# Kernel tuning notes

Hardware: AMD Instinct MI355X
Metric: run time of the kernel (lower is better)

The kernel has to match this reference:

```python
import jax, jax.numpy as jnp
import numpy as np

B, N, H, K, WIN = 512, 600, 256, 9, 129
AVG = 1.5
PAD = K // 2
PWIN = WIN + 2 * PAD  # padded window length


def setup_inputs() -> dict:
    key = jax.random.key(0)
    ks = jax.random.split(key, 8)
    tokens = jax.random.normal(ks[0], (B, N, H), dtype=jnp.float32)
    token_keys = jax.random.normal(ks[1], (B, H, N), dtype=jnp.float32)
    query = jax.random.normal(ks[2], (B, H), dtype=jnp.float32)
    num_tokens = jax.random.randint(ks[3], (B,), 300, N + 1, dtype=jnp.int32)
    tokens_mask = jnp.arange(N)[None, :] < num_tokens[:, None]
    u = jax.random.uniform(ks[4], (B,))
    window_start = (u * (num_tokens - WIN + 1).astype(jnp.float32)).astype(jnp.int32)
    alignment = jax.random.uniform(ks[5], (B, N + 2 * PAD), dtype=jnp.float32)
    cum_alignment = jax.random.uniform(ks[6], (B, N + 2 * PAD), dtype=jnp.float32) * 50.0
    conv_w = jax.random.normal(ks[7], (H, 2, K), dtype=jnp.float32) * 0.1
    conv_b = jnp.zeros((H,), dtype=jnp.float32)
    return dict(tokens=tokens, tokens_mask=tokens_mask, token_keys=token_keys,
                num_tokens=num_tokens, query=query, alignment=alignment,
                cum_alignment=cum_alignment, window_start=window_start,
                conv_w=conv_w, conv_b=conv_b)


def reference(tokens, tokens_mask, token_keys, num_tokens, query, alignment,
              cum_alignment, window_start, conv_w, conv_b):
    scale = jnp.sqrt(jnp.float32(H))
    idx = window_start[:, None] + jnp.arange(WIN)
    pidx = window_start[:, None] + jnp.arange(PWIN)        # [B, PWIN]
    mask_w = jnp.take_along_axis(tokens_mask, idx, axis=1)
    tokens_w = jnp.take_along_axis(tokens, idx[:, :, None], axis=1)
    keys_w = jnp.take_along_axis(token_keys, idx[:, None, :], axis=2)
    last_w = jnp.take_along_axis(alignment, pidx, axis=1)                  # [B, PWIN]
    cum_w = jnp.take_along_axis(cum_alignment, pidx, axis=1)               # [B, PWIN]
    position = jnp.stack([cum_w / AVG - 1.0, last_w * 2.0 - 1.0], axis=1)  # [B, 2, PWIN]
    position = jax.lax.stop_gradient(position)  # .detach() in torch
    feat = jax.lax.conv_general_dilated(position, conv_w, (1,), 'VALID',
                                        dimension_numbers=('NCH', 'OIH', 'NCH'))
    feat = feat + conv_b[None, :, None]
    keys = feat + keys_w
    score = jnp.einsum('bh,bhw->bw', query, keys) / scale
    score = jnp.where(mask_w, score, -jnp.inf)
    align_w = jax.nn.softmax(score, axis=1)
    context = jnp.einsum('bw,bwh->bh', align_w, tokens_w)                  # [B, H]
    b_idx = jnp.arange(B)[:, None]
    full_align = jnp.zeros_like(alignment).at[b_idx, idx + PAD].set(align_w)
    new_start = jnp.argmax(full_align, axis=1).astype(jnp.int32) - PWIN // 2
    new_start = jnp.maximum(window_start, new_start)
    new_start = jnp.minimum(new_start, num_tokens - WIN)
    new_start = jnp.maximum(new_start, 0)
    unpadded = full_align[:, PAD:-PAD]                                     # [B, N]
    return (context, unpadded, full_align, cum_alignment + full_align, new_start)
```

## Files before the change

kernel.cpp:

```cpp
#include <hip/hip_runtime.h>
#include <math.h>

#define BB   512
#define NN   600
#define HH   256
#define KS   9
#define WIN  129
#define PADW 4
#define PWIN 137
#define NP   608

__global__ __launch_bounds__(1024) void attn_kernel(
    const float* __restrict__ tokens,
    const float* __restrict__ token_keys,
    const int*   __restrict__ num_tokens,
    const float* __restrict__ query,
    const float* __restrict__ alignment,
    const float* __restrict__ cum_align,
    const int*   __restrict__ window_start,
    const float* __restrict__ conv_w,
    const float* __restrict__ conv_b,
    float* __restrict__ out)
{
  const int b    = blockIdx.x;
  const int t    = threadIdx.x;
  const int lane = t & 63;
  const int wv   = t >> 6;

  __shared__ float sq[HH];
  __shared__ float scw[HH * 18];
  __shared__ float scb[HH];
  __shared__ float p0[PWIN], p1[PWIN];
  __shared__ float cred[19][8];
  __shared__ float w128red[4];
  __shared__ float sqc[19];
  __shared__ float sS[8][130];
  __shared__ float salign[WIN];
  __shared__ int   cand[WIN];
  __shared__ __align__(16) float sctx[16][HH];
  __shared__ float s_m, s_sum;
  __shared__ int   s_arg;

  const int ws = window_start[b];
  const int nt = num_tokens[b];
  const float* Kb = token_keys + (size_t)b * (HH * NN);

  float qreg = 0.f;
  if (t < HH) {
    qreg = query[b * HH + t];
    sq[t] = qreg;
    scb[t] = conv_b[t];
  }
  #pragma unroll
  for (int i = 0; i < 5; ++i) {
    int j = t + i * 1024;
    if (j < HH * 18) scw[j] = conv_w[j];
  }
  if (t < PWIN) {
    p0[t] = cum_align[b * NP + ws + t] * (1.0f / 1.5f) - 1.0f;
    p1[t] = alignment[b * NP + ws + t] * 2.0f - 1.0f;
  }
  __syncthreads();

  if (t < 152) {
    const int j = t >> 3, seg = t & 7;
    const int h0 = seg * 32;
    float a = 0.f;
    if (j < 18) {
      #pragma unroll 8
      for (int h = 0; h < 32; ++h) a += sq[h0 + h] * scw[(h0 + h) * 18 + j];
    } else {
      #pragma unroll 8
      for (int h = 0; h < 32; ++h) a += sq[h0 + h] * scb[h0 + h];
    }
    cred[j][seg] = a;
  }

  if (t < HH) {
    float v = qreg * Kb[(size_t)t * NN + ws + 128];
    #pragma unroll
    for (int off = 32; off; off >>= 1) v += __shfl_xor(v, off, 64);
    if (lane == 0) w128red[wv] = v;
  }

  {
    const int hh   = wv & 7;
    const int wseg = wv >> 3;
    const int w    = wseg * 64 + lane;
    const float* Kp  = Kb + (size_t)(hh * 32) * NN + ws + w;
    const float* sqp = sq + hh * 32;
    float acc = 0.f;
    #pragma unroll 8
    for (int h = 0; h < 32; ++h) acc += sqp[h] * Kp[(size_t)h * NN];
    sS[hh][w] = acc;
  }
  __syncthreads();

  if (t < 19) {
    const float* c = cred[t];
    sqc[t] = ((c[0] + c[1]) + (c[2] + c[3])) + ((c[4] + c[5]) + (c[6] + c[7]));
  }
  __syncthreads();

  float sc = 0.f;
  if (t < WIN) {
    float dot;
    if (t < 128) {
      dot = 0.f;
      #pragma unroll
      for (int g = 0; g < 8; ++g) dot += sS[g][t];
    } else {
      dot = w128red[0] + w128red[1] + w128red[2] + w128red[3];
    }
    float f = sqc[18];
    #pragma unroll
    for (int k = 0; k < KS; ++k) f += sqc[k] * p0[t + k] + sqc[9 + k] * p1[t + k];
    sc = (dot + f) * 0.0625f;
    if (ws + t >= nt) sc = -INFINITY;
    salign[t] = sc;
  }
  __syncthreads();

  if (t < 64) {
    float m0 = fmaxf(salign[t], salign[t + 64]);
    if (t == 0) m0 = fmaxf(m0, salign[128]);
    #pragma unroll
    for (int off = 32; off; off >>= 1) m0 = fmaxf(m0, __shfl_xor(m0, off, 64));
    if (t == 0) s_m = m0;
  }
  __syncthreads();
  if (t < WIN) {
    float e = expf(sc - s_m);
    salign[t] = e;
    cand[t] = (sc == s_m) ? t : 0x7fffffff;
  }
  __syncthreads();
  if (t < 64) {
    float s0 = salign[t] + salign[t + 64] + ((t == 0) ? salign[128] : 0.f);
    int   c0 = min(cand[t], cand[t + 64]);
    if (t == 0) c0 = min(c0, cand[128]);
    #pragma unroll
    for (int off = 32; off; off >>= 1) {
      s0 += __shfl_xor(s0, off, 64);
      c0 = min(c0, __shfl_xor(c0, off, 64));
    }
    if (t == 0) { s_sum = s0; s_arg = c0; }
  }
  __syncthreads();
  const float inv = 1.0f / s_sum;
  if (t < WIN) salign[t] *= inv;
  __syncthreads();

  float* out0 = out;
  float* out1 = out0 + BB * HH;
  float* out2 = out1 + BB * NN;
  float* out3 = out2 + BB * NP;
  float* out4 = out3 + BB * NP;

  {
    const float* Tb = tokens + (size_t)b * (NN * HH) + (size_t)ws * HH;
    float4 acc = make_float4(0.f, 0.f, 0.f, 0.f);
    #pragma unroll
    for (int i = 0; i < 8; ++i) {
      const int w = wv + 16 * i;
      const float a = salign[w];
      const float4 v4 = ((const float4*)(Tb + (size_t)w * HH))[lane];
      acc.x += a * v4.x; acc.y += a * v4.y; acc.z += a * v4.z; acc.w += a * v4.w;
    }
    if (wv == 0) {
      const float a = salign[128];
      const float4 v4 = ((const float4*)(Tb + (size_t)128 * HH))[lane];
      acc.x += a * v4.x; acc.y += a * v4.y; acc.z += a * v4.z; acc.w += a * v4.w;
    }
    ((float4*)&sctx[wv][0])[lane] = acc;
  }
  __syncthreads();
  if (t < HH) {
    float c = 0.f;
    #pragma unroll
    for (int v = 0; v < 16; ++v) c += sctx[v][t];
    out0[b * HH + t] = c;
  }

  if (t < NN) {
    float v = (t >= ws && t <= ws + 128) ? salign[t - ws] : 0.f;
    out1[b * NN + t] = v;
  }
  if (t < NP) {
    float v = (t >= ws + PADW && t <= ws + PADW + 128) ? salign[t - ws - PADW] : 0.f;
    out2[b * NP + t] = v;
    out3[b * NP + t] = v + cum_align[b * NP + t];
  }
  if (t == 0) {
    int jstar = ws + PADW + s_arg;
    int ns = jstar - (PWIN / 2);
    ns = max(ws, ns);
    ns = min(ns, nt - WIN);
    ns = max(ns, 0);
    out4[b] = (float)ns;
  }
}

extern "C" void kernel_launch(void* const* d_in, const int* in_sizes, int n_in,
                              void* d_out, int out_size, void* d_ws, size_t ws_size,
                              hipStream_t stream) {
  const float* tokens       = (const float*)d_in[0];
  const float* token_keys   = (const float*)d_in[2];
  const int*   num_tokens   = (const int*)d_in[3];
  const float* query        = (const float*)d_in[4];
  const float* alignment    = (const float*)d_in[5];
  const float* cum_align    = (const float*)d_in[6];
  const int*   window_start = (const int*)d_in[7];
  const float* conv_w       = (const float*)d_in[8];
  const float* conv_b       = (const float*)d_in[9];

  attn_kernel<<<BB, 1024, 0, stream>>>(tokens, token_keys, num_tokens, query,
                                       alignment, cum_align, window_start,
                                       conv_w, conv_b, (float*)d_out);
}
```

Before: 512.1 us.

## Halve block size, drop smem conv weights, fuse softmax reductions, defer normalization

Moves from 1024-thread to 512-thread blocks with a launch bound of 512 threads and 8 blocks per CU, and redistributes the key-dot, context and output loops to match. Removes the per-block shared-memory staging of conv weights and bias, reading them straight from global memory instead, which shrinks shared memory and should allow more resident blocks. Merges the max, argmax, exp and sum steps into a single wavefront pass, removing several barriers. Applies the softmax normalization as a multiply at output time instead of a separate pass. Cumulative-alignment loads are issued early so their latency overlaps with compute. The cost is more serial work per thread and uncached global reads of conv weights per block.

```diff
diff --git a/kernel.cpp b/kernel.cpp
--- a/kernel.cpp
+++ b/kernel.cpp
@@ -10,7 +10,7 @@
 #define PWIN 137
 #define NP   608
 
-__global__ __launch_bounds__(1024) void attn_kernel(
+__global__ __launch_bounds__(512, 8) void attn_kernel(
     const float* __restrict__ tokens,
     const float* __restrict__ token_keys,
     const int*   __restrict__ num_tokens,
@@ -28,71 +28,64 @@
   const int wv   = t >> 6;
 
   __shared__ float sq[HH];
-  __shared__ float scw[HH * 18];
-  __shared__ float scb[HH];
   __shared__ float p0[PWIN], p1[PWIN];
   __shared__ float cred[19][8];
   __shared__ float w128red[4];
   __shared__ float sqc[19];
   __shared__ float sS[8][130];
   __shared__ float salign[WIN];
-  __shared__ int   cand[WIN];
-  __shared__ __align__(16) float sctx[16][HH];
-  __shared__ float s_m, s_sum;
+  __shared__ __align__(16) float sctx[8][HH];
+  __shared__ float s_sum;
   __shared__ int   s_arg;
 
   const int ws = window_start[b];
   const int nt = num_tokens[b];
-  const float* Kb = token_keys + (size_t)b * (HH * NN);
+  const float* __restrict__ Kb = token_keys + (size_t)b * (HH * NN);
+
+  const float cum0 = cum_align[b * NP + t];
+  const float cum1 = (t + 512 < NP) ? cum_align[b * NP + t + 512] : 0.f;
 
   float qreg = 0.f;
-  if (t < HH) {
-    qreg = query[b * HH + t];
-    sq[t] = qreg;
-    scb[t] = conv_b[t];
-  }
-  #pragma unroll
-  for (int i = 0; i < 5; ++i) {
-    int j = t + i * 1024;
-    if (j < HH * 18) scw[j] = conv_w[j];
-  }
+  if (t < HH) { qreg = query[b * HH + t]; sq[t] = qreg; }
   if (t < PWIN) {
     p0[t] = cum_align[b * NP + ws + t] * (1.0f / 1.5f) - 1.0f;
     p1[t] = alignment[b * NP + ws + t] * 2.0f - 1.0f;
   }
   __syncthreads();
+
+  {
+    const float* __restrict__ Kp  = Kb + (size_t)(wv * 32) * NN + ws;
+    const float* __restrict__ sqp = sq + wv * 32;
+    float a0 = 0.f, a1 = 0.f;
+    #pragma unroll 4
+    for (int h = 0; h < 32; ++h) {
+      const float q = sqp[h];
+      a0 += q * Kp[(size_t)h * NN + lane];
+      a1 += q * Kp[(size_t)h * NN + 64 + lane];
+    }
+    sS[wv][lane]      = a0;
+    sS[wv][64 + lane] = a1;
+  }
+
+  if (t < HH) {
+    float v = qreg * Kb[(size_t)t * NN + ws + 128];
+    #pragma unroll
+    for (int off = 32; off; off >>= 1) v += __shfl_xor(v, off, 64);
+    if (lane == 0) w128red[wv] = v;
+  }
 
   if (t < 152) {
     const int j = t >> 3, seg = t & 7;
     const int h0 = seg * 32;
     float a = 0.f;
     if (j < 18) {
-      #pragma unroll 8
-      for (int h = 0; h < 32; ++h) a += sq[h0 + h] * scw[(h0 + h) * 18 + j];
+      #pragma unroll 4
+      for (int h = 0; h < 32; ++h) a += sq[h0 + h] * conv_w[(h0 + h) * 18 + j];
     } else {
-      #pragma unroll 8
-      for (int h = 0; h < 32; ++h) a += sq[h0 + h] * scb[h0 + h];
+      #pragma unroll 4
+      for (int h = 0; h < 32; ++h) a += sq[h0 + h] * conv_b[h0 + h];
     }
     cred[j][seg] = a;
-  }
-
-  if (t < HH) {
-    float v = qreg * Kb[(size_t)t * NN + ws + 128];
-    #pragma unroll
-    for (int off = 32; off; off >>= 1) v += __shfl_xor(v, off, 64);
-    if (lane == 0) w128red[wv] = v;
-  }
-
-  {
-    const int hh   = wv & 7;
-    const int wseg = wv >> 3;
-    const int w    = wseg * 64 + lane;
-    const float* Kp  = Kb + (size_t)(hh * 32) * NN + ws + w;
-    const float* sqp = sq + hh * 32;
-    float acc = 0.f;
-    #pragma unroll 8
-    for (int h = 0; h < 32; ++h) acc += sqp[h] * Kp[(size_t)h * NN];
-    sS[hh][w] = acc;
   }
   __syncthreads();
 
@@ -102,7 +95,6 @@
   }
   __syncthreads();
 
-  float sc = 0.f;
   if (t < WIN) {
     float dot;
     if (t < 128) {
@@ -115,41 +107,38 @@
     float f = sqc[18];
     #pragma unroll
     for (int k = 0; k < KS; ++k) f += sqc[k] * p0[t + k] + sqc[9 + k] * p1[t + k];
-    sc = (dot + f) * 0.0625f;
+    float sc = (dot + f) * 0.0625f;
     if (ws + t >= nt) sc = -INFINITY;
     salign[t] = sc;
   }
   __syncthreads();
 
   if (t < 64) {
-    float m0 = fmaxf(salign[t], salign[t + 64]);
-    if (t == 0) m0 = fmaxf(m0, salign[128]);
-    #pragma unroll
-    for (int off = 32; off; off >>= 1) m0 = fmaxf(m0, __shfl_xor(m0, off, 64));
-    if (t == 0) s_m = m0;
-  }
-  __syncthreads();
-  if (t < WIN) {
-    float e = expf(sc - s_m);
-    salign[t] = e;
-    cand[t] = (sc == s_m) ? t : 0x7fffffff;
-  }
-  __syncthreads();
-  if (t < 64) {
-    float s0 = salign[t] + salign[t + 64] + ((t == 0) ? salign[128] : 0.f);
-    int   c0 = min(cand[t], cand[t + 64]);
-    if (t == 0) c0 = min(c0, cand[128]);
+    const float a0 = salign[t];
+    const float a1 = salign[t + 64];
+    const float a2 = (t == 0) ? salign[128] : -INFINITY;
+    float m = a0; int idx = t;
+    if (a1 > m) { m = a1; idx = t + 64; }
+    if (a2 > m) { m = a2; idx = 128; }
     #pragma unroll
     for (int off = 32; off; off >>= 1) {
-      s0 += __shfl_xor(s0, off, 64);
-      c0 = min(c0, __shfl_xor(c0, off, 64));
-    }
-    if (t == 0) { s_sum = s0; s_arg = c0; }
-  }
-  __syncthreads();
+      const float om = __shfl_xor(m, off, 64);
+      const int   oi = __shfl_xor(idx, off, 64);
+      if (om > m || (om == m && oi < idx)) { m = om; idx = oi; }
+    }
+    const float e0 = expf(a0 - m);
+    const float e1 = expf(a1 - m);
+    salign[t]      = e0;
+    salign[t + 64] = e1;
+    float s = e0 + e1;
+    if (t == 0) { const float e2 = expf(a2 - m); salign[128] = e2; s += e2; }
+    #pragma unroll
+    for (int off = 32; off; off >>= 1) s += __shfl_xor(s, off, 64);
+    if (t == 0) { s_sum = s; s_arg = idx; }
+  }
+  __syncthreads();
+
   const float inv = 1.0f / s_sum;
-  if (t < WIN) salign[t] *= inv;
-  __syncthreads();
 
   float* out0 = out;
   float* out1 = out0 + BB * HH;
@@ -158,11 +147,11 @@
   float* out4 = out3 + BB * NP;
 
   {
-    const float* Tb = tokens + (size_t)b * (NN * HH) + (size_t)ws * HH;
+    const float* __restrict__ Tb = tokens + (size_t)b * (NN * HH) + (size_t)ws * HH;
     float4 acc = make_float4(0.f, 0.f, 0.f, 0.f);
-    #pragma unroll
-    for (int i = 0; i < 8; ++i) {
-      const int w = wv + 16 * i;
+    #pragma unroll 4
+    for (int i = 0; i < 16; ++i) {
+      const int w = wv + 8 * i;
       const float a = salign[w];
       const float4 v4 = ((const float4*)(Tb + (size_t)w * HH))[lane];
       acc.x += a * v4.x; acc.y += a * v4.y; acc.z += a * v4.z; acc.w += a * v4.w;
@@ -174,22 +163,22 @@
     }
     ((float4*)&sctx[wv][0])[lane] = acc;
   }
-  __syncthreads();
-  if (t < HH) {
-    float c = 0.f;
-    #pragma unroll
-    for (int v = 0; v < 16; ++v) c += sctx[v][t];
-    out0[b * HH + t] = c;
-  }
-
-  if (t < NN) {
-    float v = (t >= ws && t <= ws + 128) ? salign[t - ws] : 0.f;
-    out1[b * NN + t] = v;
-  }
-  if (t < NP) {
-    float v = (t >= ws + PADW && t <= ws + PADW + 128) ? salign[t - ws - PADW] : 0.f;
-    out2[b * NP + t] = v;
-    out3[b * NP + t] = v + cum_align[b * NP + t];
+
+  for (int j = t; j < NN; j += 512) {
+    const float v = (j >= ws && j <= ws + 128) ? salign[j - ws] * inv : 0.f;
+    out1[b * NN + j] = v;
+  }
+  {
+    int j = t;
+    const float v0 = (j >= ws + PADW && j <= ws + PADW + 128) ? salign[j - ws - PADW] * inv : 0.f;
+    out2[b * NP + j] = v0;
+    out3[b * NP + j] = v0 + cum0;
+    j = t + 512;
+    if (j < NP) {
+      const float v1 = (j >= ws + PADW && j <= ws + PADW + 128) ? salign[j - ws - PADW] * inv : 0.f;
+      out2[b * NP + j] = v1;
+      out3[b * NP + j] = v1 + cum1;
+    }
   }
   if (t == 0) {
     int jstar = ws + PADW + s_arg;
@@ -198,6 +187,14 @@
     ns = min(ns, nt - WIN);
     ns = max(ns, 0);
     out4[b] = (float)ns;
+  }
+  __syncthreads();
+
+  if (t < HH) {
+    float c = 0.f;
+    #pragma unroll
+    for (int v = 0; v < 8; ++v) c += sctx[v][t];
+    out0[b * HH + t] = c * inv;
   }
 }
 
@@ -214,7 +211,7 @@
   const float* conv_w       = (const float*)d_in[8];
   const float* conv_b       = (const float*)d_in[9];
 
-  attn_kernel<<<BB, 1024, 0, stream>>>(tokens, token_keys, num_tokens, query,
-                                       alignment, cum_align, window_start,
-                                       conv_w, conv_b, (float*)d_out);
+  attn_kernel<<<BB, 512, 0, stream>>>(tokens, token_keys, num_tokens, query,
+                                      alignment, cum_align, window_start,
+                                      conv_w, conv_b, (float*)d_out);
 }
```

After: 515.0 us. About the same (+0.6%).
